# Performance work log

Hardware: AMD Instinct MI355X
Metric: run time of the kernel (lower is better)

The kernel has to match this reference:

```python
import jax, jax.numpy as jnp
import numpy as np

N, K, H, W = 8, 16, 256, 256
C, P = 4, 100000


def setup_inputs() -> dict:
    key = jax.random.key(0)
    k1, k2, k3, k4, k5 = jax.random.split(key, 5)
    raw_idx = jax.random.randint(k1, (N, K, H, W), 0, P, dtype=jnp.int32)
    # per-pixel number of valid points in [0, K]; trailing slots are -1 (z-sorted convention)
    cnt = jax.random.randint(k2, (N, 1, H, W), 0, K + 1, dtype=jnp.int32)
    k_ar = jnp.arange(K, dtype=jnp.int32).reshape(1, K, 1, 1)
    fragments = jnp.where(k_ar < cnt, raw_idx, -1)
    alphas = jax.random.uniform(k3, (N, K, H, W), dtype=jnp.float32)
    ptclds = jax.random.uniform(k4, (C, P), dtype=jnp.float32)  # packed rgba features
    background_color = jax.random.uniform(k5, (3,), dtype=jnp.float32)
    return {"fragments": fragments, "alphas": alphas, "ptclds": ptclds,
            "background_color": background_color}


def reference(fragments, alphas, ptclds, background_color):
    # fragments: (N,K,H,W) int32, -1 = no point; alphas: (N,K,H,W); ptclds: (C,P)
    valid = fragments >= 0
    a = jnp.where(valid, alphas, jnp.zeros((), alphas.dtype))  # skipped points contribute 0
    # front-to-back transmittance: cum_k = prod_{j<k} (1 - a_j)  (exclusive cumprod)
    cum = jnp.cumprod(1.0 - a, axis=1)
    cum_excl = jnp.concatenate([jnp.ones_like(cum[:, :1]), cum[:, :-1]], axis=1)
    wts = a * cum_excl  # (N,K,H,W)
    idx = jnp.where(valid, fragments, 0)
    feats = ptclds.T[idx]  # gather -> (N,K,H,W,C)
    images = jnp.einsum('nkhw,nkhwc->nchw', wts, feats)  # (N,C,H,W)
    # background fill where no nearest point exists
    bg = jnp.concatenate([background_color, jnp.ones((1,), background_color.dtype)])  # rgba
    bg_mask = fragments[:, 0] < 0  # (N,H,W)
    images = jnp.where(bg_mask[:, None, :, :], bg[None, :, None, None], images)
    return images
```

## Files before the change

kernel.cpp:

```cpp
#include <hip/hip_runtime.h>

#define NB 8
#define KF 16
#define HGT 256
#define WID 256
#define HW (HGT * WID)
#define NPIX (NB * HW)
#define NPTS 100000
#define NCH 4

__global__ void ptclds_transpose_kernel(const float* __restrict__ pt,
                                        float4* __restrict__ ws) {
    int p = blockIdx.x * blockDim.x + threadIdx.x;
    if (p < NPTS) {
        ws[p] = make_float4(pt[p],
                            pt[NPTS + p],
                            pt[2 * NPTS + p],
                            pt[3 * NPTS + p]);
    }
}

template <bool PACKED>
__global__ __launch_bounds__(256) void composite_kernel(
    const int* __restrict__ frags,
    const float* __restrict__ alphas,
    const float* __restrict__ pt,
    const float4* __restrict__ ws,
    const float* __restrict__ bg,
    float* __restrict__ out)
{
    int i = blockIdx.x * blockDim.x + threadIdx.x;
    if (i >= NPIX) return;

    int n  = i >> 16;
    int hw = i & (HW - 1);

    long base = (long)n * KF * HW + hw;

    float4 acc = make_float4(0.f, 0.f, 0.f, 0.f);

    int f0 = frags[base];
    if (f0 < 0) {
        acc = make_float4(bg[0], bg[1], bg[2], 1.0f);
    } else {
        float T = 1.0f;
        int f = f0;
        #pragma unroll
        for (int k = 0; k < KF; ++k) {
            float a = alphas[base + (long)k * HW];
            float w = a * T;
            float4 feat;
            if (PACKED) {
                feat = ws[f];
            } else {
                feat = make_float4(pt[f], pt[NPTS + f],
                                   pt[2 * NPTS + f], pt[3 * NPTS + f]);
            }
            acc.x += w * feat.x;
            acc.y += w * feat.y;
            acc.z += w * feat.z;
            acc.w += w * feat.w;
            T *= (1.0f - a);
            if (k + 1 < KF) {
                f = frags[base + (long)(k + 1) * HW];
                if (f < 0) break;
            }
        }
    }

    long ob = (long)n * NCH * HW + hw;
    out[ob]          = acc.x;
    out[ob + HW]     = acc.y;
    out[ob + 2 * HW] = acc.z;
    out[ob + 3 * HW] = acc.w;
}

extern "C" void kernel_launch(void* const* d_in, const int* in_sizes, int n_in,
                              void* d_out, int out_size, void* d_ws, size_t ws_size,
                              hipStream_t stream) {
    const int*   frags  = (const int*)d_in[0];
    const float* alphas = (const float*)d_in[1];
    const float* pt     = (const float*)d_in[2];
    const float* bg     = (const float*)d_in[3];
    float* out = (float*)d_out;

    const bool packed = (ws_size >= (size_t)NPTS * sizeof(float4));

    if (packed) {
        float4* ws = (float4*)d_ws;
        ptclds_transpose_kernel<<<(NPTS + 255) / 256, 256, 0, stream>>>(pt, ws);
        composite_kernel<true><<<NPIX / 256, 256, 0, stream>>>(
            frags, alphas, pt, ws, bg, out);
    } else {
        composite_kernel<false><<<NPIX / 256, 256, 0, stream>>>(
            frags, alphas, pt, (const float4*)nullptr, bg, out);
    }
}
```

Measured before the change: 127.7 us.

## Process two pixels per thread with vectorized loads and branchless masking

Each thread now composites two adjacent pixels, loading fragment indices, alphas and writing outputs as 2-wide vectors. All 16 fragment slots are prefetched into registers up front, and the early-exit break is replaced by masking invalid slots to zero weight with index 0. This aims to raise memory-level parallelism and remove divergent branching. The cost is that every alpha and gather is now fetched even for empty trailing slots, increasing memory traffic.

```diff
diff --git a/kernel.cpp b/kernel.cpp
--- a/kernel.cpp
+++ b/kernel.cpp
@@ -29,50 +29,60 @@
     const float* __restrict__ bg,
     float* __restrict__ out)
 {
-    int i = blockIdx.x * blockDim.x + threadIdx.x;
-    if (i >= NPIX) return;
+    int t = blockIdx.x * blockDim.x + threadIdx.x;
+    if (t >= NPIX / 2) return;
 
-    int n  = i >> 16;
-    int hw = i & (HW - 1);
+    int n  = t >> 15;
+    int hw = (t & 32767) << 1;
 
     long base = (long)n * KF * HW + hw;
 
-    float4 acc = make_float4(0.f, 0.f, 0.f, 0.f);
+    int2 f[KF];
+    #pragma unroll
+    for (int k = 0; k < KF; ++k)
+        f[k] = *reinterpret_cast<const int2*>(&frags[base + (long)k * HW]);
 
-    int f0 = frags[base];
-    if (f0 < 0) {
-        acc = make_float4(bg[0], bg[1], bg[2], 1.0f);
-    } else {
-        float T = 1.0f;
-        int f = f0;
-        #pragma unroll
-        for (int k = 0; k < KF; ++k) {
-            float a = alphas[base + (long)k * HW];
-            float w = a * T;
-            float4 feat;
-            if (PACKED) {
-                feat = ws[f];
-            } else {
-                feat = make_float4(pt[f], pt[NPTS + f],
-                                   pt[2 * NPTS + f], pt[3 * NPTS + f]);
-            }
-            acc.x += w * feat.x;
-            acc.y += w * feat.y;
-            acc.z += w * feat.z;
-            acc.w += w * feat.w;
-            T *= (1.0f - a);
-            if (k + 1 < KF) {
-                f = frags[base + (long)(k + 1) * HW];
-                if (f < 0) break;
-            }
+    float bg0 = bg[0], bg1 = bg[1], bg2 = bg[2];
+
+    float4 acc0 = make_float4(0.f, 0.f, 0.f, 0.f);
+    float4 acc1 = make_float4(0.f, 0.f, 0.f, 0.f);
+    float T0 = 1.0f, T1 = 1.0f;
+
+    #pragma unroll
+    for (int k = 0; k < KF; ++k) {
+        float2 a = *reinterpret_cast<const float2*>(&alphas[base + (long)k * HW]);
+        const bool v0 = f[k].x >= 0;
+        const bool v1 = f[k].y >= 0;
+        const int i0 = v0 ? f[k].x : 0;
+        const int i1 = v1 ? f[k].y : 0;
+        float4 g0, g1;
+        if (PACKED) {
+            g0 = ws[i0];
+            g1 = ws[i1];
+        } else {
+            g0 = make_float4(pt[i0], pt[NPTS + i0], pt[2*NPTS + i0], pt[3*NPTS + i0]);
+            g1 = make_float4(pt[i1], pt[NPTS + i1], pt[2*NPTS + i1], pt[3*NPTS + i1]);
         }
+        const float a0 = v0 ? a.x : 0.f;
+        const float a1 = v1 ? a.y : 0.f;
+        const float w0 = a0 * T0;
+        const float w1 = a1 * T1;
+        acc0.x += w0 * g0.x;  acc0.y += w0 * g0.y;
+        acc0.z += w0 * g0.z;  acc0.w += w0 * g0.w;
+        acc1.x += w1 * g1.x;  acc1.y += w1 * g1.y;
+        acc1.z += w1 * g1.z;  acc1.w += w1 * g1.w;
+        T0 *= (1.0f - a0);
+        T1 *= (1.0f - a1);
     }
 
+    if (f[0].x < 0) acc0 = make_float4(bg0, bg1, bg2, 1.0f);
+    if (f[0].y < 0) acc1 = make_float4(bg0, bg1, bg2, 1.0f);
+
     long ob = (long)n * NCH * HW + hw;
-    out[ob]          = acc.x;
-    out[ob + HW]     = acc.y;
-    out[ob + 2 * HW] = acc.z;
-    out[ob + 3 * HW] = acc.w;
+    *reinterpret_cast<float2*>(&out[ob])          = make_float2(acc0.x, acc1.x);
+    *reinterpret_cast<float2*>(&out[ob + HW])     = make_float2(acc0.y, acc1.y);
+    *reinterpret_cast<float2*>(&out[ob + 2 * HW]) = make_float2(acc0.z, acc1.z);
+    *reinterpret_cast<float2*>(&out[ob + 3 * HW]) = make_float2(acc0.w, acc1.w);
 }
 
 extern "C" void kernel_launch(void* const* d_in, const int* in_sizes, int n_in,
@@ -89,10 +99,10 @@
     if (packed) {
         float4* ws = (float4*)d_ws;
         ptclds_transpose_kernel<<<(NPTS + 255) / 256, 256, 0, stream>>>(pt, ws);
-        composite_kernel<true><<<NPIX / 256, 256, 0, stream>>>(
+        composite_kernel<true><<<(NPIX / 2) / 256, 256, 0, stream>>>(
             frags, alphas, pt, ws, bg, out);
     } else {
-        composite_kernel<false><<<NPIX / 256, 256, 0, stream>>>(
+        composite_kernel<false><<<(NPIX / 2) / 256, 256, 0, stream>>>(
             frags, alphas, pt, (const float4*)nullptr, bg, out);
     }
 }
```

Result: faster. 119.4 us (-6.5%).

## Preload all fragment indices and alphas, then composite without early exit

Applied to the files above, without the earlier changes.

The composite kernel now issues all 16 fragment and alpha loads up front into registers, then runs a branch-free gather loop that masks invalid slots by gathering index 0 with zero weight. This removes the serial dependency between each fragment load and the break test, so memory requests can overlap. In exchange it always reads all K alphas and performs all K gathers even for pixels with few valid points, including background pixels. It also sets a minimum-blocks hint in launch_bounds to control register use.

```diff
diff --git a/kernel.cpp b/kernel.cpp
--- a/kernel.cpp
+++ b/kernel.cpp
@@ -21,7 +21,7 @@
 }
 
 template <bool PACKED>
-__global__ __launch_bounds__(256) void composite_kernel(
+__global__ __launch_bounds__(256, 6) void composite_kernel(
     const int* __restrict__ frags,
     const float* __restrict__ alphas,
     const float* __restrict__ pt,
@@ -37,36 +37,39 @@
 
     long base = (long)n * KF * HW + hw;
 
+    int f[KF];
+    float a[KF];
+    #pragma unroll
+    for (int k = 0; k < KF; ++k)
+        f[k] = frags[base + (long)k * HW];
+    #pragma unroll
+    for (int k = 0; k < KF; ++k)
+        a[k] = alphas[base + (long)k * HW];
+
     float4 acc = make_float4(0.f, 0.f, 0.f, 0.f);
+    float T = 1.0f;
 
-    int f0 = frags[base];
-    if (f0 < 0) {
-        acc = make_float4(bg[0], bg[1], bg[2], 1.0f);
-    } else {
-        float T = 1.0f;
-        int f = f0;
-        #pragma unroll
-        for (int k = 0; k < KF; ++k) {
-            float a = alphas[base + (long)k * HW];
-            float w = a * T;
-            float4 feat;
-            if (PACKED) {
-                feat = ws[f];
-            } else {
-                feat = make_float4(pt[f], pt[NPTS + f],
-                                   pt[2 * NPTS + f], pt[3 * NPTS + f]);
-            }
-            acc.x += w * feat.x;
-            acc.y += w * feat.y;
-            acc.z += w * feat.z;
-            acc.w += w * feat.w;
-            T *= (1.0f - a);
-            if (k + 1 < KF) {
-                f = frags[base + (long)(k + 1) * HW];
-                if (f < 0) break;
-            }
+    #pragma unroll
+    for (int k = 0; k < KF; ++k) {
+        const bool v = f[k] >= 0;
+        const int idx = v ? f[k] : 0;
+        float4 g;
+        if (PACKED) {
+            g = ws[idx];
+        } else {
+            g = make_float4(pt[idx], pt[NPTS + idx],
+                            pt[2 * NPTS + idx], pt[3 * NPTS + idx]);
         }
+        const float av = v ? a[k] : 0.f;
+        const float w = av * T;
+        acc.x += w * g.x;
+        acc.y += w * g.y;
+        acc.z += w * g.z;
+        acc.w += w * g.w;
+        T *= (1.0f - av);
     }
+
+    if (f[0] < 0) acc = make_float4(bg[0], bg[1], bg[2], 1.0f);
 
     long ob = (long)n * NCH * HW + hw;
     out[ob]          = acc.x;
```

Result: faster. 115.9 us (-9.3%).
